# Kernel tuning notes

Measured on AMD Instinct MI355X. Metric: run time of the kernel, lower is better.

Reference implementation:

```python
import jax, jax.numpy as jnp
import numpy as np

B, T = 8, 512
V, H = 2048, 4
N_EMBD = 768


def setup_inputs() -> dict:
    key = jax.random.key(0)
    k1, k2, k3, k4 = jax.random.split(key, 4)
    x = jax.random.randint(k1, (B, T, 1), 0, V, dtype=jnp.int64)
    cooc = jax.random.normal(k2, (V, V, H), dtype=jnp.float32)
    proj_w = jax.random.normal(k3, (N_EMBD, V * H * H), dtype=jnp.float32) * 0.01
    proj_b = jax.random.normal(k4, (N_EMBD,), dtype=jnp.float32)
    return {"x": x, "cooc": cooc, "proj_w": proj_w, "proj_b": proj_b}


def reference(x, cooc, proj_w, proj_b):
    # x: [B,T,1] int token ids; cooc: [V,V,H]
    tok = x[..., 0]  # [B,T]
    Vv, _, Hh = cooc.shape
    Bb, Tt = tok.shape
    # att scores: wei[b,i,j,h] = cooc[tok[b,i], tok[b,j], h]  (keys index rows, queries cols)
    wei = cooc[tok[:, :, None], tok[:, None, :], :]  # [B,T,T,H]
    att = jax.nn.softmax(wei, axis=2)  # softmax over last token axis (dim=-1 of [T,T])
    att = att + jnp.eye(Tt, dtype=att.dtype)[None, :, :, None]  # self loops
    # value embedding table is flatten(cooc, 1, 2): [V, V*H]; same for every head
    v = cooc.reshape(Vv, Vv * Hh)[tok]  # [B,T,V*H]
    # per-head: att[:,:,:,h] @ v -> [B,T,V*H]; concat over heads on last dim
    out = jnp.einsum('bijh,bjd->bihd', att, v)  # [B,T,H,V*H]
    out = out.reshape(Bb, Tt, Hh * Vv * Hh)  # [B,T,H*V*H]
    # projection (dropout p=0.0 / eval mode -> identity)
    y = out @ proj_w.T + proj_b  # [B,T,n_embd]
    return y
```

## Files before the change

### kernel.cpp

```cpp
#include <hip/hip_runtime.h>
#include <stdint.h>

#define B_    8
#define T_    512
#define V_    2048
#define H_    4
#define NE_   768
#define D_    8192
#define PWROW 32768
#define M1    3072
#define K3    2048
#define MTT_E 6291456UL

typedef __attribute__((ext_vector_type(8))) short bf16x8;
typedef __attribute__((ext_vector_type(4))) float f32x4;

__device__ __forceinline__ unsigned short f2bf(float f) {
  union { float f; unsigned int u; } c; c.f = f;
  unsigned int u = c.u;
  return (unsigned short)((u + 0x7FFFu + ((u >> 16) & 1u)) >> 16);
}
__device__ __forceinline__ float bf2f(unsigned short s) {
  union { unsigned int u; float f; } c; c.u = ((unsigned int)s) << 16;
  return c.f;
}

__global__ __launch_bounds__(256) void cvt_k(
    const float* __restrict__ src, unsigned short* __restrict__ dst, int n4) {
  int i = blockIdx.x * 256 + threadIdx.x;
  const int stride = gridDim.x * 256;
  for (; i < n4; i += stride) {
    const float4 v = ((const float4*)src)[i];
    ushort4 o;
    o.x = f2bf(v.x); o.y = f2bf(v.y); o.z = f2bf(v.z); o.w = f2bf(v.w);
    ((ushort4*)dst)[i] = o;
  }
}

__global__ __launch_bounds__(256) void gemm1f_k(
    const unsigned short* __restrict__ Aq,
    const unsigned short* __restrict__ Bq,
    unsigned short* __restrict__ P,
    int kk) {
  __shared__ unsigned short As[128 * 32];
  __shared__ unsigned short Bs[128 * 32];
  const int r0 = blockIdx.x * 128;
  const int t0 = blockIdx.y * 128;
  const int z  = blockIdx.z;
  const int kbeg = z * kk, kend = kbeg + kk;
  const int tid  = threadIdx.x;
  const int lane = tid & 63, wave = tid >> 6;
  const int wr = wave >> 1, wc = wave & 1;
  const int fr = lane & 15, fq = lane >> 4;
  const int l4 = lane >> 2, lb = lane & 3;
  unsigned short* __restrict__ Pz = P + (size_t)z * MTT_E;

  f32x4 acc[4][4];
  #pragma unroll
  for (int m = 0; m < 4; ++m)
    #pragma unroll
    for (int n = 0; n < 4; ++n) acc[m][n] = (f32x4){0.f, 0.f, 0.f, 0.f};

  for (int k0 = kbeg; k0 < kend; k0 += 32) {
    __syncthreads();
    #pragma unroll
    for (int c = 0; c < 2; ++c) {
      const int ch  = wave * 2 + c;
      const int row = ch * 16 + l4;
      __builtin_amdgcn_global_load_lds(
          (const __attribute__((address_space(1))) void*)
              (Aq + (size_t)(r0 + row) * D_ + k0 + lb * 8),
          (__attribute__((address_space(3))) void*)(As + ch * 512),
          16, 0, 0);
      __builtin_amdgcn_global_load_lds(
          (const __attribute__((address_space(1))) void*)
              (Bq + (size_t)(t0 + row) * D_ + k0 + lb * 8),
          (__attribute__((address_space(3))) void*)(Bs + ch * 512),
          16, 0, 0);
    }
    __syncthreads();
    bf16x8 af[4], bf[4];
    #pragma unroll
    for (int m = 0; m < 4; ++m)
      af[m] = *(const bf16x8*)&As[(wr * 64 + m * 16 + fr) * 32 + fq * 8];
    #pragma unroll
    for (int n = 0; n < 4; ++n)
      bf[n] = *(const bf16x8*)&Bs[(wc * 64 + n * 16 + fr) * 32 + fq * 8];
    #pragma unroll
    for (int m = 0; m < 4; ++m)
      #pragma unroll
      for (int n = 0; n < 4; ++n)
        acc[m][n] = __builtin_amdgcn_mfma_f32_16x16x32_bf16(af[m], bf[n], acc[m][n], 0, 0, 0);
  }

  #pragma unroll
  for (int m = 0; m < 4; ++m)
    #pragma unroll
    for (int n = 0; n < 4; ++n) {
      const int rbase = r0 + wr * 64 + m * 16 + fq * 4;
      const int t = t0 + wc * 64 + n * 16 + fr;
      ushort4 o;
      o.x = f2bf(acc[m][n][0]); o.y = f2bf(acc[m][n][1]);
      o.z = f2bf(acc[m][n][2]); o.w = f2bf(acc[m][n][3]);
      *(ushort4*)&Pz[(size_t)(rbase >> 2) * D_ + t * H_] = o;
    }
}

__global__ __launch_bounds__(256) void reduceN_k(
    unsigned short* __restrict__ P0, int nz) {
  const size_t i = ((size_t)blockIdx.x * 256 + threadIdx.x) * 8;
  float s[8];
  {
    ushort4 a0 = *(const ushort4*)(P0 + i);
    ushort4 a1 = *(const ushort4*)(P0 + i + 4);
    s[0] = bf2f(a0.x); s[1] = bf2f(a0.y); s[2] = bf2f(a0.z); s[3] = bf2f(a0.w);
    s[4] = bf2f(a1.x); s[5] = bf2f(a1.y); s[6] = bf2f(a1.z); s[7] = bf2f(a1.w);
  }
  for (int z = 1; z < nz; ++z) {
    const unsigned short* Pz = P0 + (size_t)z * MTT_E;
    ushort4 b0 = *(const ushort4*)(Pz + i);
    ushort4 b1 = *(const ushort4*)(Pz + i + 4);
    s[0] += bf2f(b0.x); s[1] += bf2f(b0.y); s[2] += bf2f(b0.z); s[3] += bf2f(b0.w);
    s[4] += bf2f(b1.x); s[5] += bf2f(b1.y); s[6] += bf2f(b1.z); s[7] += bf2f(b1.w);
  }
  ushort4 o0, o1;
  o0.x = f2bf(s[0]); o0.y = f2bf(s[1]); o0.z = f2bf(s[2]); o0.w = f2bf(s[3]);
  o1.x = f2bf(s[4]); o1.y = f2bf(s[5]); o1.z = f2bf(s[6]); o1.w = f2bf(s[7]);
  *(ushort4*)(P0 + i) = o0;
  *(ushort4*)(P0 + i + 4) = o1;
}

__global__ __launch_bounds__(256) void gather_k(
    const unsigned short* __restrict__ mtT, const int* __restrict__ x,
    unsigned short* __restrict__ GT) {
  __shared__ int toks[B_ * T_];
  const int tid = threadIdx.x;
  #pragma unroll
  for (int c = 0; c < 16; ++c) toks[c * 256 + tid] = x[c * 256 + tid];
  __syncthreads();

  const int lane = tid & 63, wave = tid >> 6;
  const int e = blockIdx.x * 4 + wave;
  const unsigned short* mrow = mtT + (size_t)e * D_;
  #pragma unroll
  for (int b = 0; b < B_; ++b) {
    unsigned short* grow = GT + ((size_t)b * NE_ + e) * K3;
    const int* tb = toks + b * T_;
    #pragma unroll
    for (int r = 0; r < 8; ++r) {
      const int j = r * 64 + lane;
      const uint2 v = *(const uint2*)(mrow + (size_t)tb[j] * H_);
      *(uint2*)(grow + j * H_) = v;
    }
  }
}

__global__ __launch_bounds__(256) void gemm3f_k(
    const unsigned short* __restrict__ att,
    const unsigned short* __restrict__ GT,
    const float* __restrict__ bias,
    float* __restrict__ y) {
  __shared__ unsigned short As[128 * 32];
  __shared__ unsigned short Bs[64 * 32];
  const int b  = blockIdx.z;
  const int i0 = blockIdx.x * 128;
  const int e0 = blockIdx.y * 64;
  const int tid  = threadIdx.x;
  const int lane = tid & 63, wave = tid >> 6;
  const int wr = wave >> 1, wc = wave & 1;
  const int fr = lane & 15, fq = lane >> 4;

  f32x4 acc[4][2];
  #pragma unroll
  for (int m = 0; m < 4; ++m)
    #pragma unroll
    for (int n = 0; n < 2; ++n) acc[m][n] = (f32x4){0.f, 0.f, 0.f, 0.f};

  const unsigned short* aB = att + (size_t)(b * T_ + i0) * K3;
  const unsigned short* bB = GT + ((size_t)b * NE_ + e0) * K3;

  for (int k0 = 0; k0 < K3; k0 += 32) {
    __syncthreads();
    #pragma unroll
    for (int rdi = 0; rdi < 2; ++rdi) {
      const int q = rdi * 256 + tid;
      const int row = q >> 2, koff = (q & 3) * 8;
      __builtin_amdgcn_global_load_lds(
          (const __attribute__((address_space(1))) void*)
              (aB + (size_t)row * K3 + k0 + koff),
          (__attribute__((address_space(3))) void*)(As + q * 8),
          16, 0, 0);
    }
    {
      const int q = tid;
      const int row = q >> 2, koff = (q & 3) * 8;
      __builtin_amdgcn_global_load_lds(
          (const __attribute__((address_space(1))) void*)
              (bB + (size_t)row * K3 + k0 + koff),
          (__attribute__((address_space(3))) void*)(Bs + q * 8),
          16, 0, 0);
    }
    __syncthreads();
    bf16x8 af[4], bf[2];
    #pragma unroll
    for (int m = 0; m < 4; ++m)
      af[m] = *(const bf16x8*)&As[(wr * 64 + m * 16 + fr) * 32 + fq * 8];
    #pragma unroll
    for (int n = 0; n < 2; ++n)
      bf[n] = *(const bf16x8*)&Bs[(wc * 32 + n * 16 + fr) * 32 + fq * 8];
    #pragma unroll
    for (int m = 0; m < 4; ++m)
      #pragma unroll
      for (int n = 0; n < 2; ++n)
        acc[m][n] = __builtin_amdgcn_mfma_f32_16x16x32_bf16(af[m], bf[n], acc[m][n], 0, 0, 0);
  }

  #pragma unroll
  for (int m = 0; m < 4; ++m)
    #pragma unroll
    for (int n = 0; n < 2; ++n) {
      const int i = i0 + wr * 64 + m * 16 + fq * 4;
      const int e = e0 + wc * 32 + n * 16 + fr;
      const float be = bias[e];
      #pragma unroll
      for (int g = 0; g < 4; ++g)
        y[(size_t)(b * T_ + i + g) * NE_ + e] = acc[m][n][g] + be;
    }
}

__global__ __launch_bounds__(64) void softmax_k(
    const int* __restrict__ x, const float* __restrict__ cooc,
    unsigned short* __restrict__ att) {
  const int bi = blockIdx.x;
  const int b = bi >> 9, i = bi & (T_ - 1);
  const int lane = threadIdx.x;
  const int ti = x[b * T_ + i];
  const float* crow = cooc + (size_t)ti * D_;

  float w[8][4];
  #pragma unroll
  for (int r = 0; r < 8; ++r) {
    const int j = lane + r * 64;
    const int tj = x[b * T_ + j];
    const float4 v = *(const float4*)(crow + (size_t)tj * H_);
    w[r][0] = v.x; w[r][1] = v.y; w[r][2] = v.z; w[r][3] = v.w;
  }
  float m[4] = {-1e30f, -1e30f, -1e30f, -1e30f};
  #pragma unroll
  for (int r = 0; r < 8; ++r)
    #pragma unroll
    for (int h = 0; h < 4; ++h) m[h] = fmaxf(m[h], w[r][h]);
  #pragma unroll
  for (int off = 32; off > 0; off >>= 1)
    #pragma unroll
    for (int h = 0; h < 4; ++h) m[h] = fmaxf(m[h], __shfl_xor(m[h], off));
  float s[4] = {0.f, 0.f, 0.f, 0.f};
  #pragma unroll
  for (int r = 0; r < 8; ++r)
    #pragma unroll
    for (int h = 0; h < 4; ++h) { w[r][h] = __expf(w[r][h] - m[h]); s[h] += w[r][h]; }
  #pragma unroll
  for (int off = 32; off > 0; off >>= 1)
    #pragma unroll
    for (int h = 0; h < 4; ++h) s[h] += __shfl_xor(s[h], off);
  float inv[4];
  #pragma unroll
  for (int h = 0; h < 4; ++h) inv[h] = 1.f / s[h];

  unsigned short* arow = att + (size_t)(b * T_ + i) * (T_ * H_);
  #pragma unroll
  for (int r = 0; r < 8; ++r) {
    const int j = lane + r * 64;
    const float d = (j == i) ? 1.f : 0.f;
    ushort4 o;
    o.x = f2bf(w[r][0] * inv[0] + d);
    o.y = f2bf(w[r][1] * inv[1] + d);
    o.z = f2bf(w[r][2] * inv[2] + d);
    o.w = f2bf(w[r][3] * inv[3] + d);
    *(ushort4*)(arow + (size_t)j * H_) = o;
  }
}

__global__ __launch_bounds__(256) void gemm1_k(
    const float* __restrict__ pw, const float* __restrict__ cooc,
    unsigned short* __restrict__ mtT) {
  __shared__ unsigned short As[128 * 32];
  __shared__ unsigned short Bs[64 * 32];
  const int h  = blockIdx.z;
  const int e0 = blockIdx.x * 128;
  const int t0 = blockIdx.y * 64;
  const int tid  = threadIdx.x;
  const int lane = tid & 63, wave = tid >> 6;
  const int wr = wave >> 1, wc = wave & 1;
  const int fr = lane & 15, fq = lane >> 4;

  f32x4 acc[4][2];
  #pragma unroll
  for (int m = 0; m < 4; ++m)
    #pragma unroll
    for (int n = 0; n < 2; ++n) acc[m][n] = (f32x4){0.f, 0.f, 0.f, 0.f};

  const float* aB = pw + (size_t)e0 * PWROW + (size_t)h * D_;
  const float* bB = cooc + (size_t)t0 * D_;

  for (int k0 = 0; k0 < D_; k0 += 32) {
    __syncthreads();
    #pragma unroll
    for (int c = 0; c < 4; ++c) {
      const int fe = (c * 256 + tid) * 4;
      const int row = fe >> 5, k = fe & 31;
      const float4 v = *(const float4*)(aB + (size_t)row * PWROW + k0 + k);
      ushort4 o; o.x = f2bf(v.x); o.y = f2bf(v.y); o.z = f2bf(v.z); o.w = f2bf(v.w);
      *(ushort4*)&As[fe] = o;
    }
    #pragma unroll
    for (int c = 0; c < 2; ++c) {
      const int fe = (c * 256 + tid) * 4;
      const int row = fe >> 5, k = fe & 31;
      const float4 v = *(const float4*)(bB + (size_t)row * D_ + k0 + k);
      ushort4 o; o.x = f2bf(v.x); o.y = f2bf(v.y); o.z = f2bf(v.z); o.w = f2bf(v.w);
      *(ushort4*)&Bs[fe] = o;
    }
    __syncthreads();
    bf16x8 af[4], bf[2];
    #pragma unroll
    for (int m = 0; m < 4; ++m)
      af[m] = *(const bf16x8*)&As[(wr * 64 + m * 16 + fr) * 32 + fq * 8];
    #pragma unroll
    for (int n = 0; n < 2; ++n)
      bf[n] = *(const bf16x8*)&Bs[(wc * 32 + n * 16 + fr) * 32 + fq * 8];
    #pragma unroll
    for (int m = 0; m < 4; ++m)
      #pragma unroll
      for (int n = 0; n < 2; ++n)
        acc[m][n] = __builtin_amdgcn_mfma_f32_16x16x32_bf16(af[m], bf[n], acc[m][n], 0, 0, 0);
  }

  #pragma unroll
  for (int m = 0; m < 4; ++m)
    #pragma unroll
    for (int n = 0; n < 2; ++n) {
      const int e = e0 + wr * 64 + m * 16 + fq * 4;
      const int t = t0 + wc * 32 + n * 16 + fr;
      #pragma unroll
      for (int g = 0; g < 4; ++g)
        mtT[(size_t)(e + g) * D_ + t * H_ + h] = f2bf(acc[m][n][g]);
    }
}

__global__ __launch_bounds__(256) void gemm3_k(
    const unsigned short* __restrict__ att, const unsigned short* __restrict__ mtT,
    const int* __restrict__ x, const float* __restrict__ bias,
    float* __restrict__ y) {
  __shared__ unsigned short As[64 * 32];
  __shared__ unsigned short Bs[128 * 32];
  const int b  = blockIdx.z;
  const int i0 = blockIdx.x * 64;
  const int e0 = blockIdx.y * 128;
  const int tid  = threadIdx.x;
  const int lane = tid & 63, wave = tid >> 6;
  const int wr = wave >> 1, wc = wave & 1;
  const int fr = lane & 15, fq = lane >> 4;

  f32x4 acc[2][4];
  #pragma unroll
  for (int m = 0; m < 2; ++m)
    #pragma unroll
    for (int n = 0; n < 4; ++n) acc[m][n] = (f32x4){0.f, 0.f, 0.f, 0.f};

  const unsigned short* aB = att + (size_t)(b * T_ + i0) * (T_ * H_);

  for (int ks = 0; ks < 64; ++ks) {
    const int k0 = ks * 32;
    __syncthreads();
    {
      const int fe = tid * 8;
      const int row = fe >> 5, k = fe & 31;
      const uint4 v = *(const uint4*)(aB + (size_t)row * (T_ * H_) + k0 + k);
      *(uint4*)&As[fe] = v;
    }
    #pragma unroll
    for (int c = 0; c < 4; ++c) {
      const int q = c * 256 + tid;
      const int n = q >> 3, j8 = q & 7;
      const int tj = x[b * T_ + ks * 8 + j8];
      const uint2 v = *(const uint2*)(mtT + (size_t)(e0 + n) * D_ + tj * H_);
      *(uint2*)&Bs[n * 32 + j8 * 4] = v;
    }
    __syncthreads();
    bf16x8 af[2], bf[4];
    #pragma unroll
    for (int m = 0; m < 2; ++m)
      af[m] = *(const bf16x8*)&As[(wr * 32 + m * 16 + fr) * 32 + fq * 8];
    #pragma unroll
    for (int n = 0; n < 4; ++n)
      bf[n] = *(const bf16x8*)&Bs[(wc * 64 + n * 16 + fr) * 32 + fq * 8];
    #pragma unroll
    for (int m = 0; m < 2; ++m)
      #pragma unroll
      for (int n = 0; n < 4; ++n)
        acc[m][n] = __builtin_amdgcn_mfma_f32_16x16x32_bf16(af[m], bf[n], acc[m][n], 0, 0, 0);
  }

  #pragma unroll
  for (int m = 0; m < 2; ++m)
    #pragma unroll
    for (int n = 0; n < 4; ++n) {
      const int i = i0 + wr * 32 + m * 16 + fq * 4;
      const int e = e0 + wc * 64 + n * 16 + fr;
      const float be = bias[e];
      #pragma unroll
      for (int g = 0; g < 4; ++g)
        y[(size_t)(b * T_ + i + g) * NE_ + e] = acc[m][n][g] + be;
    }
}

extern "C" void kernel_launch(void* const* d_in, const int* in_sizes, int n_in,
                              void* d_out, int out_size, void* d_ws, size_t ws_size,
                              hipStream_t stream) {
  const int*   x    = (const int*)d_in[0];
  const float* cooc = (const float*)d_in[1];
  const float* pw   = (const float*)d_in[2];
  const float* pb   = (const float*)d_in[3];
  float* y = (float*)d_out;

  const size_t BQ_E = (size_t)V_ * D_;
  const size_t AQ_E = (size_t)M1 * D_;

  unsigned short* mtT = (unsigned short*)d_ws;

  int nz = 0;
  for (int c = 4; c >= 1; c >>= 1) {
    if (ws_size >= ((size_t)c * MTT_E + BQ_E + AQ_E) * 2) { nz = c; break; }
  }

  if (nz >= 1) {
    unsigned short* Bq  = mtT + (size_t)nz * MTT_E;
    unsigned short* Aq  = Bq + BQ_E;
    unsigned short* GT  = Bq;
    unsigned short* att = Aq;
    hipLaunchKernelGGL(cvt_k, dim3(2048), dim3(256), 0, stream,
                       pw, Aq, (int)(AQ_E / 4));
    hipLaunchKernelGGL(cvt_k, dim3(2048), dim3(256), 0, stream,
                       cooc, Bq, (int)(BQ_E / 4));
    hipLaunchKernelGGL(gemm1f_k, dim3(M1 / 128, V_ / 128, nz), dim3(256), 0, stream,
                       Aq, Bq, mtT, D_ / nz);
    if (nz > 1)
      hipLaunchKernelGGL(reduceN_k, dim3((unsigned)(MTT_E / (256 * 8))), dim3(256),
                         0, stream, mtT, nz);
    hipLaunchKernelGGL(softmax_k, dim3(B_ * T_), dim3(64), 0, stream, x, cooc, att);
    hipLaunchKernelGGL(gather_k, dim3(NE_ / 4), dim3(256), 0, stream, mtT, x, GT);
    hipLaunchKernelGGL(gemm3f_k, dim3(T_ / 128, NE_ / 64, B_), dim3(256), 0, stream,
                       att, GT, pb, y);
  } else {
    unsigned short* att = mtT + MTT_E;
    hipLaunchKernelGGL(gemm1_k, dim3(NE_ / 128, V_ / 64, H_), dim3(256), 0, stream,
                       pw, cooc, mtT);
    hipLaunchKernelGGL(softmax_k, dim3(B_ * T_), dim3(64), 0, stream, x, cooc, att);
    hipLaunchKernelGGL(gemm3_k, dim3(T_ / 64, NE_ / 128, B_), dim3(256), 0, stream,
                       att, mtT, x, pb, y);
  }
}
```

Baseline: 265.0 us.

## Add double-buffered 256x256 swizzled GEMM1 kernel and fuse conversion launches

Adds a new projection GEMM kernel with 256x256 tiles, 512 threads, K-tiles of 64 and double-buffered LDS with an XOR swizzle, so global-to-LDS loads overlap MFMA work and LDS bank conflicts drop. The two fp32-to-bf16 conversion launches are merged into one kernel. When the workspace allows, split-K is raised to 8, which adds partial-sum traffic for the reduce kernel but keeps enough blocks in flight for the larger tiles. The 128 KB LDS per block and heavy register use limit occupancy.

```diff
diff --git a/kernel.cpp b/kernel.cpp
--- a/kernel.cpp
+++ b/kernel.cpp
@@ -25,23 +25,146 @@
   return c.f;
 }
 
-__global__ __launch_bounds__(256) void cvt_k(
-    const float* __restrict__ src, unsigned short* __restrict__ dst, int n4) {
+__global__ __launch_bounds__(256) void cvtAB_k(
+    const float* __restrict__ cooc, const float* __restrict__ pw,
+    unsigned short* __restrict__ dst, int bq4, int n4) {
   int i = blockIdx.x * 256 + threadIdx.x;
   const int stride = gridDim.x * 256;
   for (; i < n4; i += stride) {
-    const float4 v = ((const float4*)src)[i];
+    const float4 v = (i < bq4) ? ((const float4*)cooc)[i]
+                               : ((const float4*)pw)[i - bq4];
     ushort4 o;
     o.x = f2bf(v.x); o.y = f2bf(v.y); o.z = f2bf(v.z); o.w = f2bf(v.w);
     ((ushort4*)dst)[i] = o;
   }
 }
 
+__global__ __launch_bounds__(512, 2) void gemm1p_k(
+    const unsigned short* __restrict__ Aq,
+    const unsigned short* __restrict__ Bq,
+    unsigned short* __restrict__ P,
+    int kk_per) {
+  __shared__ unsigned short lds[2][2][256 * 64];
+  const int r0 = blockIdx.x * 256;
+  const int t0 = blockIdx.y * 256;
+  const int z  = blockIdx.z;
+  const int kbeg = z * kk_per;
+  const int NT = kk_per / 64;
+  const int tid  = threadIdx.x;
+  const int lane = tid & 63, w = tid >> 6;
+  const int wm = w >> 2, wn = w & 3;
+  const int fr = lane & 15, fq = lane >> 4;
+  unsigned short* __restrict__ Pz = P + (size_t)z * MTT_E;
+
+  f32x4 acc[8][4];
+  #pragma unroll
+  for (int m = 0; m < 8; ++m)
+    #pragma unroll
+    for (int n = 0; n < 4; ++n) acc[m][n] = (f32x4){0.f, 0.f, 0.f, 0.f};
+
+  auto STAGE = [&](int d, int k0) {
+    #pragma unroll
+    for (int i = 0; i < 4; ++i) {
+      const int q   = (w * 4 + i) * 64 + lane;
+      const int row = q >> 3;
+      const int c16 = (q & 7) ^ (row & 7);
+      __builtin_amdgcn_global_load_lds(
+          (const __attribute__((address_space(1))) void*)
+              (Aq + (size_t)(r0 + row) * D_ + k0 + c16 * 8),
+          (__attribute__((address_space(3))) void*)(&lds[d][0][(w * 4 + i) * 512]),
+          16, 0, 0);
+    }
+    #pragma unroll
+    for (int i = 0; i < 4; ++i) {
+      const int q   = (w * 4 + i) * 64 + lane;
+      const int row = q >> 3;
+      const int c16 = (q & 7) ^ (row & 7);
+      __builtin_amdgcn_global_load_lds(
+          (const __attribute__((address_space(1))) void*)
+              (Bq + (size_t)(t0 + row) * D_ + k0 + c16 * 8),
+          (__attribute__((address_space(3))) void*)(&lds[d][1][(w * 4 + i) * 512]),
+          16, 0, 0);
+    }
+  };
+  #define OFFS(r, c) ((r) * 64 + (((c) ^ ((r) & 7)) * 8))
+
+  STAGE(0, kbeg);
+
+  for (int kt = 0; kt < NT; ++kt) {
+    if (kt + 1 < NT) {
+      STAGE((kt + 1) & 1, kbeg + (kt + 1) * 64);
+      asm volatile("s_waitcnt vmcnt(8)" ::: "memory");
+    } else {
+      asm volatile("s_waitcnt vmcnt(0)" ::: "memory");
+    }
+    __builtin_amdgcn_s_barrier();
+    __builtin_amdgcn_sched_barrier(0);
+
+    const unsigned short* Ab = &lds[kt & 1][0][0];
+    const unsigned short* Bb = &lds[kt & 1][1][0];
+
+    bf16x8 afA[4][2], afB[4][2], bf0[2][2], bf1[2][2];
+    #pragma unroll
+    for (int m = 0; m < 4; ++m)
+      #pragma unroll
+      for (int kk = 0; kk < 2; ++kk)
+        afA[m][kk] = *(const bf16x8*)&Ab[OFFS(wm * 128 + m * 16 + fr, kk * 4 + fq)];
+    #pragma unroll
+    for (int n = 0; n < 2; ++n)
+      #pragma unroll
+      for (int kk = 0; kk < 2; ++kk) {
+        bf0[n][kk] = *(const bf16x8*)&Bb[OFFS(wn * 64 + n * 16 + fr, kk * 4 + fq)];
+        bf1[n][kk] = *(const bf16x8*)&Bb[OFFS(wn * 64 + 32 + n * 16 + fr, kk * 4 + fq)];
+      }
+
+    __builtin_amdgcn_s_setprio(1);
+    #pragma unroll
+    for (int m = 0; m < 4; ++m)
+      #pragma unroll
+      for (int n = 0; n < 2; ++n)
+        #pragma unroll
+        for (int kk = 0; kk < 2; ++kk) {
+          acc[m][n]     = __builtin_amdgcn_mfma_f32_16x16x32_bf16(afA[m][kk], bf0[n][kk], acc[m][n], 0, 0, 0);
+          acc[m][n + 2] = __builtin_amdgcn_mfma_f32_16x16x32_bf16(afA[m][kk], bf1[n][kk], acc[m][n + 2], 0, 0, 0);
+        }
+    #pragma unroll
+    for (int m = 0; m < 4; ++m)
+      #pragma unroll
+      for (int kk = 0; kk < 2; ++kk)
+        afB[m][kk] = *(const bf16x8*)&Ab[OFFS(wm * 128 + 64 + m * 16 + fr, kk * 4 + fq)];
+    #pragma unroll
+    for (int m = 0; m < 4; ++m)
+      #pragma unroll
+      for (int n = 0; n < 2; ++n)
+        #pragma unroll
+        for (int kk = 0; kk < 2; ++kk) {
+          acc[m + 4][n]     = __builtin_amdgcn_mfma_f32_16x16x32_bf16(afB[m][kk], bf0[n][kk], acc[m + 4][n], 0, 0, 0);
+          acc[m + 4][n + 2] = __builtin_amdgcn_mfma_f32_16x16x32_bf16(afB[m][kk], bf1[n][kk], acc[m + 4][n + 2], 0, 0, 0);
+        }
+    __builtin_amdgcn_s_setprio(0);
+
+    __builtin_amdgcn_s_barrier();
+    __builtin_amdgcn_sched_barrier(0);
+  }
+  #undef OFFS
+
+  #pragma unroll
+  for (int m = 0; m < 8; ++m)
+    #pragma unroll
+    for (int n = 0; n < 4; ++n) {
+      const int rbase = r0 + wm * 128 + m * 16 + fq * 4;
+      const int t = t0 + wn * 64 + n * 16 + fr;
+      ushort4 o;
+      o.x = f2bf(acc[m][n][0]); o.y = f2bf(acc[m][n][1]);
+      o.z = f2bf(acc[m][n][2]); o.w = f2bf(acc[m][n][3]);
+      *(ushort4*)&Pz[(size_t)(rbase >> 2) * D_ + t * H_] = o;
+    }
+}
+
 __global__ __launch_bounds__(256) void gemm1f_k(
     const unsigned short* __restrict__ Aq,
     const unsigned short* __restrict__ Bq,
-    unsigned short* __restrict__ P,
-    int kk) {
+    unsigned short* __restrict__ P, int kk) {
   __shared__ unsigned short As[128 * 32];
   __shared__ unsigned short Bs[128 * 32];
   const int r0 = blockIdx.x * 128;
@@ -70,13 +193,11 @@
       __builtin_amdgcn_global_load_lds(
           (const __attribute__((address_space(1))) void*)
               (Aq + (size_t)(r0 + row) * D_ + k0 + lb * 8),
-          (__attribute__((address_space(3))) void*)(As + ch * 512),
-          16, 0, 0);
+          (__attribute__((address_space(3))) void*)(As + ch * 512), 16, 0, 0);
       __builtin_amdgcn_global_load_lds(
           (const __attribute__((address_space(1))) void*)
               (Bq + (size_t)(t0 + row) * D_ + k0 + lb * 8),
-          (__attribute__((address_space(3))) void*)(Bs + ch * 512),
-          16, 0, 0);
+          (__attribute__((address_space(3))) void*)(Bs + ch * 512), 16, 0, 0);
     }
     __syncthreads();
     bf16x8 af[4], bf[4];
@@ -92,7 +213,6 @@
       for (int n = 0; n < 4; ++n)
         acc[m][n] = __builtin_amdgcn_mfma_f32_16x16x32_bf16(af[m], bf[n], acc[m][n], 0, 0, 0);
   }
-
   #pragma unroll
   for (int m = 0; m < 4; ++m)
     #pragma unroll
@@ -188,8 +308,7 @@
       __builtin_amdgcn_global_load_lds(
           (const __attribute__((address_space(1))) void*)
               (aB + (size_t)row * K3 + k0 + koff),
-          (__attribute__((address_space(3))) void*)(As + q * 8),
-          16, 0, 0);
+          (__attribute__((address_space(3))) void*)(As + q * 8), 16, 0, 0);
     }
     {
       const int q = tid;
@@ -197,8 +316,7 @@
       __builtin_amdgcn_global_load_lds(
           (const __attribute__((address_space(1))) void*)
               (bB + (size_t)row * K3 + k0 + koff),
-          (__attribute__((address_space(3))) void*)(Bs + q * 8),
-          16, 0, 0);
+          (__attribute__((address_space(3))) void*)(Bs + q * 8), 16, 0, 0);
     }
     __syncthreads();
     bf16x8 af[4], bf[2];
@@ -335,7 +453,6 @@
       for (int n = 0; n < 2; ++n)
         acc[m][n] = __builtin_amdgcn_mfma_f32_16x16x32_bf16(af[m], bf[n], acc[m][n], 0, 0, 0);
   }
-
   #pragma unroll
   for (int m = 0; m < 4; ++m)
     #pragma unroll
@@ -401,7 +518,6 @@
       for (int n = 0; n < 4; ++n)
         acc[m][n] = __builtin_amdgcn_mfma_f32_16x16x32_bf16(af[m], bf[n], acc[m][n], 0, 0, 0);
   }
-
   #pragma unroll
   for (int m = 0; m < 2; ++m)
     #pragma unroll
@@ -428,23 +544,27 @@
   const size_t AQ_E = (size_t)M1 * D_;
 
   unsigned short* mtT = (unsigned short*)d_ws;
-
-  int nz = 0;
-  for (int c = 4; c >= 1; c >>= 1) {
-    if (ws_size >= ((size_t)c * MTT_E + BQ_E + AQ_E) * 2) { nz = c; break; }
-  }
+  auto need = [&](int c) { return ((size_t)c * MTT_E + BQ_E + AQ_E) * 2; };
+
+  int nz = 0, pipe = 0;
+  if      (ws_size >= need(8)) { nz = 8; pipe = 1; }
+  else if (ws_size >= need(4)) { nz = 4; pipe = 1; }
+  else if (ws_size >= need(2)) { nz = 2; pipe = 0; }
+  else if (ws_size >= need(1)) { nz = 1; pipe = 0; }
 
   if (nz >= 1) {
     unsigned short* Bq  = mtT + (size_t)nz * MTT_E;
     unsigned short* Aq  = Bq + BQ_E;
     unsigned short* GT  = Bq;
     unsigned short* att = Aq;
-    hipLaunchKernelGGL(cvt_k, dim3(2048), dim3(256), 0, stream,
-                       pw, Aq, (int)(AQ_E / 4));
-    hipLaunchKernelGGL(cvt_k, dim3(2048), dim3(256), 0, stream,
-                       cooc, Bq, (int)(BQ_E / 4));
-    hipLaunchKernelGGL(gemm1f_k, dim3(M1 / 128, V_ / 128, nz), dim3(256), 0, stream,
-                       Aq, Bq, mtT, D_ / nz);
+    hipLaunchKernelGGL(cvtAB_k, dim3(2048), dim3(256), 0, stream,
+                       cooc, pw, Bq, (int)(BQ_E / 4), (int)((BQ_E + AQ_E) / 4));
+    if (pipe)
+      hipLaunchKernelGGL(gemm1p_k, dim3(M1 / 256, V_ / 256, nz), dim3(512), 0,
+                         stream, Aq, Bq, mtT, D_ / nz);
+    else
+      hipLaunchKernelGGL(gemm1f_k, dim3(M1 / 128, V_ / 128, nz), dim3(256), 0,
+                         stream, Aq, Bq, mtT, D_ / nz);
     if (nz > 1)
       hipLaunchKernelGGL(reduceN_k, dim3((unsigned)(MTT_E / (256 * 8))), dim3(256),
                          0, stream, mtT, nz);
```

Result: faster. 242.1 us (-8.7%).
